# Kernel tuning notes

Measured on AMD Instinct MI355X. Metric: run time of the kernel, lower is better.

Reference implementation:

```python
import jax, jax.numpy as jnp
import numpy as np

EPS = 1e-5
F_BIAS = 1.0
KEEP_H = 0.7
KEEP_C = 0.7


def _block_layernorm(x, gamma, beta, n_blocks, h):
    # Normalize each of the n_blocks chunks of width h independently,
    # then apply a single per-feature gain/bias of size n_blocks*h.
    B = x.shape[0]
    xb = x.reshape(B, n_blocks, h)
    mean = jnp.mean(xb, axis=-1, keepdims=True)
    var = jnp.mean(jnp.square(xb - mean), axis=-1, keepdims=True)
    xn = (xb - mean) * jax.lax.rsqrt(var + EPS)
    return xn.reshape(B, n_blocks * h) * gamma + beta


def setup_inputs() -> dict:
    key = jax.random.key(0)
    ks = jax.random.split(key, 7)
    B, X, H = 65536, 256, 256
    x = jax.random.normal(ks[0], (B, X), dtype=jnp.float32)
    h = jax.random.normal(ks[1], (B, H), dtype=jnp.float32)
    c = jax.random.normal(ks[2], (B, H), dtype=jnp.float32)
    # orthogonal-initializer stand-in: scaled gaussian
    W_full = jax.random.normal(ks[3], (X + H, 4 * H), dtype=jnp.float32) / np.sqrt(X + H)
    bias = jnp.zeros((4 * H,), dtype=jnp.float32)
    g1 = jnp.ones((4 * H,), dtype=jnp.float32)
    b1 = jnp.zeros((4 * H,), dtype=jnp.float32)
    g2 = jnp.ones((H,), dtype=jnp.float32)
    b2 = jnp.zeros((H,), dtype=jnp.float32)
    mask_h = jax.random.uniform(ks[4], (B, H), dtype=jnp.float32)
    mask_c = jax.random.uniform(ks[5], (B, H), dtype=jnp.float32)
    return {"x": x, "h": h, "c": c, "W_full": W_full, "bias": bias,
            "g1": g1, "b1": b1, "g2": g2, "b2": b2,
            "mask_h": mask_h, "mask_c": mask_c}


def reference(x, h, c, W_full, bias, g1, b1, g2, b2, mask_h, mask_c):
    H = h.shape[1]
    concat = jnp.concatenate([x, h], axis=1) @ W_full + bias       # [B, 4H]
    concat = _block_layernorm(concat, g1, b1, 4, H)
    i, j, f, o = jnp.split(concat, 4, axis=1)
    new_c = c * jax.nn.sigmoid(f + F_BIAS) + jax.nn.sigmoid(i) * jnp.tanh(j)
    new_c = _block_layernorm(new_c, g2, b2, 1, H)
    new_h = jnp.tanh(new_c) * jax.nn.sigmoid(o)
    # zoneout: keep the NEW state with prob keep, else carry over old state
    mh = (mask_h < KEEP_H).astype(new_h.dtype)
    mc = (mask_c < KEEP_C).astype(new_c.dtype)
    new_h = mh * new_h + (1.0 - mh) * h
    new_c = mc * new_c + (1.0 - mc) * c
    return (new_h, new_c)
```

## Files before the change

kernel.cpp:

```cpp
#include <hip/hip_runtime.h>


#define NTHREADS 512
#define TILE_M 64
#define PRE_STRIDE 20

typedef _Float16 half8 __attribute__((ext_vector_type(8)));
typedef _Float16 half4v __attribute__((ext_vector_type(4)));
typedef float float4v __attribute__((ext_vector_type(4)));

__device__ __forceinline__ void async16(const void* g, void* l) {
  __builtin_amdgcn_global_load_lds(
      (const __attribute__((address_space(1))) unsigned int*)g,
      (__attribute__((address_space(3))) unsigned int*)l, 16, 0, 0);
}

__device__ __forceinline__ float sigm(float x) {
  return __fdividef(1.0f, 1.0f + __expf(-x));
}
__device__ __forceinline__ float tanh_fast(float x) {
  return 2.0f * __fdividef(1.0f, 1.0f + __expf(-2.0f * x)) - 1.0f;
}

__global__ __launch_bounds__(256) void wt_kernel(const float* __restrict__ W,
                                                 _Float16* __restrict__ Wt) {
  __shared__ float tile[64][65];
  const int bn = blockIdx.x << 6;
  const int bk = blockIdx.y << 6;
  const int tid = threadIdx.x;
#pragma unroll
  for (int i = 0; i < 16; ++i) {
    int idx = (i << 8) + tid;
    int kk = idx >> 6, nn = idx & 63;
    tile[kk][nn] = W[(size_t)(bk + kk) * 1024 + bn + nn];
  }
  __syncthreads();
#pragma unroll
  for (int i = 0; i < 16; ++i) {
    int idx = (i << 8) + tid;
    int nn = idx >> 6, kk = idx & 63;
    Wt[(size_t)(bn + nn) * 512 + bk + kk] = (_Float16)tile[kk][nn];
  }
}

__global__ __launch_bounds__(NTHREADS, 2) void lstm_fused(
    const float* __restrict__ x, const float* __restrict__ hin,
    const float* __restrict__ cin, const _Float16* __restrict__ Wt,
    const float* __restrict__ bias, const float* __restrict__ g1,
    const float* __restrict__ b1, const float* __restrict__ g2,
    const float* __restrict__ b2, const float* __restrict__ mhp,
    const float* __restrict__ mcp, float* __restrict__ out) {
  extern __shared__ char smem[];
  _Float16* abuf = (_Float16*)smem;
  _Float16* wbuf0 = (_Float16*)(smem + 4096);
  _Float16* wbuf1 = (_Float16*)(smem + 36864);
  _Float16* preT = (_Float16*)smem;

  const int tid = threadIdx.x;
  const int wave = tid >> 6;
  const int lane = tid & 63;
  const int l15 = lane & 15;
  const int quad = lane >> 4;
  const int blockRow = blockIdx.x * TILE_M;

  float4v acc[4][8];
#pragma unroll
  for (int s = 0; s < 4; ++s)
#pragma unroll
    for (int c = 0; c < 8; ++c) acc[s][c] = (float4v){0.f, 0.f, 0.f, 0.f};

  const int arow = tid >> 3;
  const int ap4 = (tid & 7) << 2;
  const float* xrow = x + (size_t)(blockRow + arow) * 256 + ap4;
  const float* hrow = hin + (size_t)(blockRow + arow) * 256 + ap4;
  const int aswz = (arow ^ (arow >> 2)) & 3;
  _Float16* adst = abuf + arow * 32 + (((ap4 >> 3) ^ aswz) << 3) + (ap4 & 4);

  const int wnl0 = tid >> 2;
  const int wj = (tid & 3) ^ ((wnl0 ^ (wnl0 >> 2)) & 3);
  const char* wg = (const char*)Wt + (size_t)wnl0 * 1024 + wj * 16;
  char* wl0 = (char*)wbuf0 + tid * 16;
  char* wl1 = (char*)wbuf1 + tid * 16;

  const int aslot = quad ^ ((l15 ^ (l15 >> 2)) & 3);

  {
    float4 v = *(const float4*)xrow;
    half4v hv = {(_Float16)v.x, (_Float16)v.y, (_Float16)v.z, (_Float16)v.w};
    *(half4v*)adst = hv;
  }
#pragma unroll
  for (int it = 0; it < 4; ++it) async16(wg + it * 131072, wl0 + it * 8192);
  __syncthreads();

  float4 av;
  for (int i = 0; i < 16; ++i) {
#pragma unroll
    for (int it = 0; it < 4; ++it)
      async16(wg + 524288 + it * 131072 + i * 64, wl1 + it * 8192);
    if (i < 15) {
      const float* s1 = (i + 1 < 8) ? (xrow + (i + 1) * 32) : (hrow + (i - 7) * 32);
      av = *(const float4*)s1;
    }
    half8 af[4];
#pragma unroll
    for (int s = 0; s < 4; ++s)
      af[s] = *(const half8*)(abuf + (s * 16 + l15) * 32 + aslot * 8);
    {
      half8 bf[4];
#pragma unroll
      for (int cc = 0; cc < 4; ++cc)
        bf[cc] = *(const half8*)(wbuf0 + (wave * 64 + cc * 16 + l15) * 32 + aslot * 8);
      __builtin_amdgcn_s_setprio(1);
#pragma unroll
      for (int s = 0; s < 4; ++s)
#pragma unroll
        for (int cc = 0; cc < 4; ++cc)
          acc[s][cc] = __builtin_amdgcn_mfma_f32_16x16x32_f16(af[s], bf[cc], acc[s][cc], 0, 0, 0);
      __builtin_amdgcn_s_setprio(0);
    }
    __syncthreads();

    if (i < 15) {
#pragma unroll
      for (int it = 0; it < 4; ++it)
        async16(wg + it * 131072 + (i + 1) * 64, wl0 + it * 8192);
    }
    {
      half8 bf[4];
#pragma unroll
      for (int cc = 0; cc < 4; ++cc)
        bf[cc] = *(const half8*)(wbuf1 + (wave * 64 + cc * 16 + l15) * 32 + aslot * 8);
      __builtin_amdgcn_s_setprio(1);
#pragma unroll
      for (int s = 0; s < 4; ++s)
#pragma unroll
        for (int cc = 0; cc < 4; ++cc)
          acc[s][4 + cc] =
              __builtin_amdgcn_mfma_f32_16x16x32_f16(af[s], bf[cc], acc[s][4 + cc], 0, 0, 0);
      __builtin_amdgcn_s_setprio(0);
    }
    if (i < 15) {
      half4v hv = {(_Float16)av.x, (_Float16)av.y, (_Float16)av.z, (_Float16)av.w};
      *(half4v*)adst = hv;
    }
    __syncthreads();
  }

  float* out_h = out;
  float* out_c = out + (size_t)65536 * 256;
  const int er = tid >> 5;
  const int et = tid & 31;

#pragma unroll
  for (int p = 0; p < 4; ++p) {
    __syncthreads();
#pragma unroll
    for (int c = 0; c < 8; ++c) {
      int n = ((c >> 2) << 9) + wave * 64 + ((c & 3) << 4) + l15;
      float4v a = acc[p][c];
      half4v hv = {(_Float16)a.x, (_Float16)a.y, (_Float16)a.z, (_Float16)a.w};
      *(half4v*)(preT + n * PRE_STRIDE + (quad << 2)) = hv;
    }
    __syncthreads();

    const int rg = blockRow + (p << 4) + er;
    float mean1[4], rstd1[4];
#pragma unroll
    for (int ch = 0; ch < 4; ++ch) {
      float s = 0.f, q = 0.f;
#pragma unroll
      for (int ss = 0; ss < 8; ++ss) {
        int n = (ch << 8) + (ss << 5) + et;
        float v = (float)preT[n * PRE_STRIDE + er] + bias[n];
        s += v;
        q += v * v;
      }
#pragma unroll
      for (int m = 1; m < 32; m <<= 1) {
        s += __shfl_xor(s, m, 32);
        q += __shfl_xor(q, m, 32);
      }
      float mu = s * (1.0f / 256.0f);
      mean1[ch] = mu;
      rstd1[ch] = __frsqrt_rn(q * (1.0f / 256.0f) - mu * mu + 1e-5f);
    }

    float ncp[8], so[8], cv[8];
    float s2 = 0.f, q2 = 0.f;
#pragma unroll
    for (int ss = 0; ss < 8; ++ss) {
      int hc = (ss << 5) + et;
      float iv = ((float)preT[(hc)*PRE_STRIDE + er] + bias[hc] - mean1[0]) * rstd1[0] * g1[hc] + b1[hc];
      float jv = ((float)preT[(256 + hc) * PRE_STRIDE + er] + bias[256 + hc] - mean1[1]) * rstd1[1] * g1[256 + hc] + b1[256 + hc];
      float fv = ((float)preT[(512 + hc) * PRE_STRIDE + er] + bias[512 + hc] - mean1[2]) * rstd1[2] * g1[512 + hc] + b1[512 + hc];
      float ov = ((float)preT[(768 + hc) * PRE_STRIDE + er] + bias[768 + hc] - mean1[3]) * rstd1[3] * g1[768 + hc] + b1[768 + hc];
      float cval = cin[(size_t)rg * 256 + hc];
      float nc = cval * sigm(fv + 1.0f) + sigm(iv) * tanh_fast(jv);
      ncp[ss] = nc;
      so[ss] = sigm(ov);
      cv[ss] = cval;
      s2 += nc;
      q2 += nc * nc;
    }
#pragma unroll
    for (int m = 1; m < 32; m <<= 1) {
      s2 += __shfl_xor(s2, m, 32);
      q2 += __shfl_xor(q2, m, 32);
    }
    float mu2 = s2 * (1.0f / 256.0f);
    float rstd2 = __frsqrt_rn(q2 * (1.0f / 256.0f) - mu2 * mu2 + 1e-5f);
#pragma unroll
    for (int ss = 0; ss < 8; ++ss) {
      int hc = (ss << 5) + et;
      size_t gi = (size_t)rg * 256 + hc;
      float ncn = (ncp[ss] - mu2) * rstd2 * g2[hc] + b2[hc];
      float nh = tanh_fast(ncn) * so[ss];
      float hval = hin[gi];
      out_h[gi] = (mhp[gi] < 0.7f) ? nh : hval;
      out_c[gi] = (mcp[gi] < 0.7f) ? ncn : cv[ss];
    }
  }
}

extern "C" void kernel_launch(void* const* d_in, const int* in_sizes, int n_in,
                              void* d_out, int out_size, void* d_ws, size_t ws_size,
                              hipStream_t stream) {
  (void)in_sizes; (void)n_in; (void)out_size; (void)ws_size;
  const float* x = (const float*)d_in[0];
  const float* h = (const float*)d_in[1];
  const float* c = (const float*)d_in[2];
  const float* W = (const float*)d_in[3];
  const float* bias = (const float*)d_in[4];
  const float* g1 = (const float*)d_in[5];
  const float* b1 = (const float*)d_in[6];
  const float* g2 = (const float*)d_in[7];
  const float* b2 = (const float*)d_in[8];
  const float* mh = (const float*)d_in[9];
  const float* mc = (const float*)d_in[10];
  _Float16* Wt = (_Float16*)d_ws;

  wt_kernel<<<dim3(16, 8), dim3(256), 0, stream>>>(W, Wt);
  lstm_fused<<<dim3(1024), dim3(NTHREADS), 69632, stream>>>(
      x, h, c, Wt, bias, g1, b1, g2, b2, mh, mc, (float*)d_out);
}
```

Before: 480.6 us.

## Load weight fragments directly to registers and double-buffer A tile

Weight operands for the MFMA now come straight from global memory (L2-resident fp16 Wt) into registers, prefetched one step ahead, instead of being staged through LDS with async global-to-LDS copies. The A tile is double-buffered in LDS so each K step needs only one barrier, and the barriers wait only on LDS counters. The epilogue adds bias before the fp16 conversion, swizzles the preT writes to cut bank conflicts, and keeps gamma/beta in LDS. The cost is more VGPR pressure and a reliance on L2 bandwidth for the weight reads, and LDS use drops.

```diff
diff --git a/kernel.cpp b/kernel.cpp
--- a/kernel.cpp
+++ b/kernel.cpp
@@ -9,17 +9,14 @@
 typedef _Float16 half4v __attribute__((ext_vector_type(4)));
 typedef float float4v __attribute__((ext_vector_type(4)));
 
-__device__ __forceinline__ void async16(const void* g, void* l) {
-  __builtin_amdgcn_global_load_lds(
-      (const __attribute__((address_space(1))) unsigned int*)g,
-      (__attribute__((address_space(3))) unsigned int*)l, 16, 0, 0);
-}
-
 __device__ __forceinline__ float sigm(float x) {
   return __fdividef(1.0f, 1.0f + __expf(-x));
 }
 __device__ __forceinline__ float tanh_fast(float x) {
   return 2.0f * __fdividef(1.0f, 1.0f + __expf(-2.0f * x)) - 1.0f;
+}
+__device__ __forceinline__ void bar_lgkm() {
+  asm volatile("s_waitcnt lgkmcnt(0)\ns_barrier" ::: "memory");
 }
 
 __global__ __launch_bounds__(256) void wt_kernel(const float* __restrict__ W,
@@ -52,9 +49,11 @@
     const float* __restrict__ mcp, float* __restrict__ out) {
   extern __shared__ char smem[];
   _Float16* abuf = (_Float16*)smem;
-  _Float16* wbuf0 = (_Float16*)(smem + 4096);
-  _Float16* wbuf1 = (_Float16*)(smem + 36864);
   _Float16* preT = (_Float16*)smem;
+  float* g1l = (float*)(smem + 40960);
+  float* b1l = (float*)(smem + 45056);
+  float* g2l = (float*)(smem + 49152);
+  float* b2l = (float*)(smem + 50176);
 
   const int tid = threadIdx.x;
   const int wave = tid >> 6;
@@ -63,6 +62,15 @@
   const int quad = lane >> 4;
   const int blockRow = blockIdx.x * TILE_M;
 
+  g1l[tid] = g1[tid];
+  g1l[tid + 512] = g1[tid + 512];
+  b1l[tid] = b1[tid];
+  b1l[tid + 512] = b1[tid + 512];
+  if (tid < 256) {
+    g2l[tid] = g2[tid];
+    b2l[tid] = b2[tid];
+  }
+
   float4v acc[4][8];
 #pragma unroll
   for (int s = 0; s < 4; ++s)
@@ -73,96 +81,111 @@
   const int ap4 = (tid & 7) << 2;
   const float* xrow = x + (size_t)(blockRow + arow) * 256 + ap4;
   const float* hrow = hin + (size_t)(blockRow + arow) * 256 + ap4;
-  const int aswz = (arow ^ (arow >> 2)) & 3;
-  _Float16* adst = abuf + arow * 32 + (((ap4 >> 3) ^ aswz) << 3) + (ap4 & 4);
-
-  const int wnl0 = tid >> 2;
-  const int wj = (tid & 3) ^ ((wnl0 ^ (wnl0 >> 2)) & 3);
-  const char* wg = (const char*)Wt + (size_t)wnl0 * 1024 + wj * 16;
-  char* wl0 = (char*)wbuf0 + tid * 16;
-  char* wl1 = (char*)wbuf1 + tid * 16;
-
+  _Float16* adst =
+      abuf + arow * 32 + (((ap4 >> 3) ^ ((arow ^ (arow >> 2)) & 3)) << 3) + (ap4 & 4);
   const int aslot = quad ^ ((l15 ^ (l15 >> 2)) & 3);
+
+  const _Float16* wbase = Wt + ((size_t)(wave * 64 + l15) << 9) + (quad << 3);
 
   {
     float4 v = *(const float4*)xrow;
-    half4v hv = {(_Float16)v.x, (_Float16)v.y, (_Float16)v.z, (_Float16)v.w};
-    *(half4v*)adst = hv;
-  }
-#pragma unroll
-  for (int it = 0; it < 4; ++it) async16(wg + it * 131072, wl0 + it * 8192);
-  __syncthreads();
-
-  float4 av;
-  for (int i = 0; i < 16; ++i) {
-#pragma unroll
-    for (int it = 0; it < 4; ++it)
-      async16(wg + 524288 + it * 131072 + i * 64, wl1 + it * 8192);
-    if (i < 15) {
-      const float* s1 = (i + 1 < 8) ? (xrow + (i + 1) * 32) : (hrow + (i - 7) * 32);
-      av = *(const float4*)s1;
-    }
+    *(half4v*)adst = (half4v){(_Float16)v.x, (_Float16)v.y, (_Float16)v.z, (_Float16)v.w};
+  }
+  half8 B0[4];
+#pragma unroll
+  for (int cc = 0; cc < 4; ++cc) B0[cc] = *(const half8*)(wbase + cc * 8192);
+  float4 av1 = *(const float4*)(xrow + 32);
+  bar_lgkm();
+
+#pragma unroll 2
+  for (int i = 0; i < 15; ++i) {
+    float4 av2;
+    if (i < 14) {
+      const float* s2p = (i + 2 < 8) ? (xrow + (i + 2) * 32) : (hrow + (i - 6) * 32);
+      av2 = *(const float4*)s2p;
+    }
+    half8 B1[4];
+#pragma unroll
+    for (int cc = 0; cc < 4; ++cc)
+      B1[cc] = *(const half8*)(wbase + cc * 8192 + 262144 + i * 32);
+    const _Float16* abr = abuf + ((i & 1) << 11);
     half8 af[4];
 #pragma unroll
     for (int s = 0; s < 4; ++s)
-      af[s] = *(const half8*)(abuf + (s * 16 + l15) * 32 + aslot * 8);
+      af[s] = *(const half8*)(abr + (s * 16 + l15) * 32 + aslot * 8);
+    __builtin_amdgcn_s_setprio(1);
+#pragma unroll
+    for (int s = 0; s < 4; ++s)
+#pragma unroll
+      for (int cc = 0; cc < 4; ++cc)
+        acc[s][cc] = __builtin_amdgcn_mfma_f32_16x16x32_f16(af[s], B0[cc], acc[s][cc], 0, 0, 0);
+    __builtin_amdgcn_s_setprio(0);
+    half8 B0n[4];
+#pragma unroll
+    for (int cc = 0; cc < 4; ++cc)
+      B0n[cc] = *(const half8*)(wbase + cc * 8192 + (i + 1) * 32);
+    __builtin_amdgcn_s_setprio(1);
+#pragma unroll
+    for (int s = 0; s < 4; ++s)
+#pragma unroll
+      for (int cc = 0; cc < 4; ++cc)
+        acc[s][4 + cc] =
+            __builtin_amdgcn_mfma_f32_16x16x32_f16(af[s], B1[cc], acc[s][4 + cc], 0, 0, 0);
+    __builtin_amdgcn_s_setprio(0);
     {
-      half8 bf[4];
-#pragma unroll
-      for (int cc = 0; cc < 4; ++cc)
-        bf[cc] = *(const half8*)(wbuf0 + (wave * 64 + cc * 16 + l15) * 32 + aslot * 8);
-      __builtin_amdgcn_s_setprio(1);
-#pragma unroll
-      for (int s = 0; s < 4; ++s)
-#pragma unroll
-        for (int cc = 0; cc < 4; ++cc)
-          acc[s][cc] = __builtin_amdgcn_mfma_f32_16x16x32_f16(af[s], bf[cc], acc[s][cc], 0, 0, 0);
-      __builtin_amdgcn_s_setprio(0);
-    }
-    __syncthreads();
-
-    if (i < 15) {
-#pragma unroll
-      for (int it = 0; it < 4; ++it)
-        async16(wg + it * 131072 + (i + 1) * 64, wl0 + it * 8192);
-    }
-    {
-      half8 bf[4];
-#pragma unroll
-      for (int cc = 0; cc < 4; ++cc)
-        bf[cc] = *(const half8*)(wbuf1 + (wave * 64 + cc * 16 + l15) * 32 + aslot * 8);
-      __builtin_amdgcn_s_setprio(1);
-#pragma unroll
-      for (int s = 0; s < 4; ++s)
-#pragma unroll
-        for (int cc = 0; cc < 4; ++cc)
-          acc[s][4 + cc] =
-              __builtin_amdgcn_mfma_f32_16x16x32_f16(af[s], bf[cc], acc[s][4 + cc], 0, 0, 0);
-      __builtin_amdgcn_s_setprio(0);
-    }
-    if (i < 15) {
-      half4v hv = {(_Float16)av.x, (_Float16)av.y, (_Float16)av.z, (_Float16)av.w};
-      *(half4v*)adst = hv;
-    }
-    __syncthreads();
+      half4v hv = {(_Float16)av1.x, (_Float16)av1.y, (_Float16)av1.z, (_Float16)av1.w};
+      *(half4v*)(adst + (((i + 1) & 1) << 11)) = hv;
+    }
+    if (i < 14) av1 = av2;
+#pragma unroll
+    for (int cc = 0; cc < 4; ++cc) B0[cc] = B0n[cc];
+    bar_lgkm();
+  }
+  {
+    half8 B1[4];
+#pragma unroll
+    for (int cc = 0; cc < 4; ++cc)
+      B1[cc] = *(const half8*)(wbase + cc * 8192 + 262144 + 15 * 32);
+    const _Float16* abr = abuf + ((15 & 1) << 11);
+    half8 af[4];
+#pragma unroll
+    for (int s = 0; s < 4; ++s)
+      af[s] = *(const half8*)(abr + (s * 16 + l15) * 32 + aslot * 8);
+    __builtin_amdgcn_s_setprio(1);
+#pragma unroll
+    for (int s = 0; s < 4; ++s)
+#pragma unroll
+      for (int cc = 0; cc < 4; ++cc)
+        acc[s][cc] = __builtin_amdgcn_mfma_f32_16x16x32_f16(af[s], B0[cc], acc[s][cc], 0, 0, 0);
+#pragma unroll
+    for (int s = 0; s < 4; ++s)
+#pragma unroll
+      for (int cc = 0; cc < 4; ++cc)
+        acc[s][4 + cc] =
+            __builtin_amdgcn_mfma_f32_16x16x32_f16(af[s], B1[cc], acc[s][4 + cc], 0, 0, 0);
+    __builtin_amdgcn_s_setprio(0);
   }
 
   float* out_h = out;
   float* out_c = out + (size_t)65536 * 256;
   const int er = tid >> 5;
   const int et = tid & 31;
+  const int ro = er ^ (((et >> 4) & 1) << 1);
 
 #pragma unroll
   for (int p = 0; p < 4; ++p) {
-    __syncthreads();
+    bar_lgkm();
 #pragma unroll
     for (int c = 0; c < 8; ++c) {
       int n = ((c >> 2) << 9) + wave * 64 + ((c & 3) << 4) + l15;
+      float bn = bias[n];
       float4v a = acc[p][c];
-      half4v hv = {(_Float16)a.x, (_Float16)a.y, (_Float16)a.z, (_Float16)a.w};
+      _Float16 e0 = (_Float16)(a.x + bn), e1 = (_Float16)(a.y + bn);
+      _Float16 e2 = (_Float16)(a.z + bn), e3 = (_Float16)(a.w + bn);
+      half4v hv = (c & 1) ? (half4v){e2, e3, e0, e1} : (half4v){e0, e1, e2, e3};
       *(half4v*)(preT + n * PRE_STRIDE + (quad << 2)) = hv;
     }
-    __syncthreads();
+    bar_lgkm();
 
     const int rg = blockRow + (p << 4) + er;
     float mean1[4], rstd1[4];
@@ -172,7 +195,7 @@
 #pragma unroll
       for (int ss = 0; ss < 8; ++ss) {
         int n = (ch << 8) + (ss << 5) + et;
-        float v = (float)preT[n * PRE_STRIDE + er] + bias[n];
+        float v = (float)preT[n * PRE_STRIDE + ro];
         s += v;
         q += v * v;
       }
@@ -191,10 +214,10 @@
 #pragma unroll
     for (int ss = 0; ss < 8; ++ss) {
       int hc = (ss << 5) + et;
-      float iv = ((float)preT[(hc)*PRE_STRIDE + er] + bias[hc] - mean1[0]) * rstd1[0] * g1[hc] + b1[hc];
-      float jv = ((float)preT[(256 + hc) * PRE_STRIDE + er] + bias[256 + hc] - mean1[1]) * rstd1[1] * g1[256 + hc] + b1[256 + hc];
-      float fv = ((float)preT[(512 + hc) * PRE_STRIDE + er] + bias[512 + hc] - mean1[2]) * rstd1[2] * g1[512 + hc] + b1[512 + hc];
-      float ov = ((float)preT[(768 + hc) * PRE_STRIDE + er] + bias[768 + hc] - mean1[3]) * rstd1[3] * g1[768 + hc] + b1[768 + hc];
+      float iv = ((float)preT[(hc)*PRE_STRIDE + ro] - mean1[0]) * rstd1[0] * g1l[hc] + b1l[hc];
+      float jv = ((float)preT[(256 + hc) * PRE_STRIDE + ro] - mean1[1]) * rstd1[1] * g1l[256 + hc] + b1l[256 + hc];
+      float fv = ((float)preT[(512 + hc) * PRE_STRIDE + ro] - mean1[2]) * rstd1[2] * g1l[512 + hc] + b1l[512 + hc];
+      float ov = ((float)preT[(768 + hc) * PRE_STRIDE + ro] - mean1[3]) * rstd1[3] * g1l[768 + hc] + b1l[768 + hc];
       float cval = cin[(size_t)rg * 256 + hc];
       float nc = cval * sigm(fv + 1.0f) + sigm(iv) * tanh_fast(jv);
       ncp[ss] = nc;
@@ -214,7 +237,7 @@
     for (int ss = 0; ss < 8; ++ss) {
       int hc = (ss << 5) + et;
       size_t gi = (size_t)rg * 256 + hc;
-      float ncn = (ncp[ss] - mu2) * rstd2 * g2[hc] + b2[hc];
+      float ncn = (ncp[ss] - mu2) * rstd2 * g2l[hc] + b2l[hc];
       float nh = tanh_fast(ncn) * so[ss];
       float hval = hin[gi];
       out_h[gi] = (mhp[gi] < 0.7f) ? nh : hval;
@@ -241,6 +264,6 @@
   _Float16* Wt = (_Float16*)d_ws;
 
   wt_kernel<<<dim3(16, 8), dim3(256), 0, stream>>>(W, Wt);
-  lstm_fused<<<dim3(1024), dim3(NTHREADS), 69632, stream>>>(
+  lstm_fused<<<dim3(1024), dim3(NTHREADS), 51200, stream>>>(
       x, h, c, Wt, bias, g1, b1, g2, b2, mh, mc, (float*)d_out);
 }
```

New measurement: 509.6 us. +6.0%, slower.
